# Kernel optimization log

Measured on AMD Instinct MI355X. Metric: run time of the kernel, lower is better.

The kernel has to match this reference:

```python
import jax, jax.numpy as jnp
import numpy as np

EMBED_DIM = 768
NUM_HEADS = 8
HEAD_DIM = EMBED_DIM // NUM_HEADS


def setup_inputs() -> dict:
    key = jax.random.key(0)
    ks = jax.random.split(key, 10)
    B, N_m, N_p = 8, 1024, 1024
    s = 1.0 / np.sqrt(EMBED_DIM)
    inp = {
        "mammo_tokens": jax.random.normal(ks[0], (B, N_m, EMBED_DIM), jnp.float32),
        "patho_tokens": jax.random.normal(ks[1], (B, N_p, EMBED_DIM), jnp.float32),
        "q_w": jax.random.uniform(ks[2], (EMBED_DIM, EMBED_DIM), jnp.float32, -s, s),
        "q_b": jax.random.uniform(ks[3], (EMBED_DIM,), jnp.float32, -s, s),
        "k_w": jax.random.uniform(ks[4], (EMBED_DIM, EMBED_DIM), jnp.float32, -s, s),
        "k_b": jax.random.uniform(ks[5], (EMBED_DIM,), jnp.float32, -s, s),
        "v_w": jax.random.uniform(ks[6], (EMBED_DIM, EMBED_DIM), jnp.float32, -s, s),
        "v_b": jax.random.uniform(ks[7], (EMBED_DIM,), jnp.float32, -s, s),
        "o_w": jax.random.uniform(ks[8], (EMBED_DIM, EMBED_DIM), jnp.float32, -s, s),
        "o_b": jax.random.uniform(ks[9], (EMBED_DIM,), jnp.float32, -s, s),
    }
    return inp


def reference(mammo_tokens, patho_tokens, q_w, q_b, k_w, k_b, v_w, v_b, o_w, o_b):
    B, N_m, E = mammo_tokens.shape
    N_p = patho_tokens.shape[1]
    H, D = NUM_HEADS, HEAD_DIM
    # torch Linear: y = x @ W^T + b
    Q = (mammo_tokens @ q_w.T + q_b).reshape(B, N_m, H, D)
    K = (patho_tokens @ k_w.T + k_b).reshape(B, N_p, H, D)
    V = (patho_tokens @ v_w.T + v_b).reshape(B, N_p, H, D)
    # scores: [B, H, N_m, N_p]
    scores = jnp.einsum("bmhd,bphd->bhmp", Q, K) / np.sqrt(D).astype(jnp.float32)
    attn = jax.nn.softmax(scores, axis=-1)  # dropout omitted (eval mode)
    attended = jnp.einsum("bhmp,bphd->bmhd", attn, V).reshape(B, N_m, E)
    attended = attended @ o_w.T + o_b
    attn_avg = attn.mean(axis=1)  # [B, N_m, N_p]
    return attended, attn_avg
```

## Files before the change

kernel.cpp:

```cpp
#include <hip/hip_runtime.h>

typedef short short4v __attribute__((ext_vector_type(4)));
typedef short short8 __attribute__((ext_vector_type(8)));
typedef float f32x4 __attribute__((ext_vector_type(4)));

__device__ __forceinline__ f32x4 mfma16(short8 a, short8 b, f32x4 c) {
    return __builtin_amdgcn_mfma_f32_16x16x32_bf16(a, b, c, 0, 0, 0);
}
__device__ __forceinline__ short f2bs(float f) {
    __bf16 h = (__bf16)f;
    return __builtin_bit_cast(short, h);
}
__device__ __forceinline__ void gld_lds16(const void* g, void* l) {
    __builtin_amdgcn_global_load_lds(
        (const __attribute__((address_space(1))) void*)g,
        (__attribute__((address_space(3))) void*)l, 16, 0, 0);
}

__global__ __launch_bounds__(256) void cvt_b16(const float* __restrict__ in,
                                               short* __restrict__ out) {
    const size_t i = ((size_t)blockIdx.x * 256 + threadIdx.x) * 8;
    const float4 v0 = *(const float4*)(in + i);
    const float4 v1 = *(const float4*)(in + i + 4);
    short8 s;
    s[0] = f2bs(v0.x); s[1] = f2bs(v0.y); s[2] = f2bs(v0.z); s[3] = f2bs(v0.w);
    s[4] = f2bs(v1.x); s[5] = f2bs(v1.y); s[6] = f2bs(v1.z); s[7] = f2bs(v1.w);
    *(short8*)(out + i) = s;
}

__global__ __launch_bounds__(256) void gemm_bw(const short* __restrict__ A,
                                               const short* __restrict__ Wb,
                                               const float* __restrict__ bias,
                                               void* __restrict__ Cv,
                                               int mode) {
    __shared__ short sBuf[2][128][64];

    const int tid = threadIdx.x;
    const int wave = tid >> 6, lane = tid & 63;
    const int quad = lane >> 4, l16 = lane & 15;
    const int n0 = blockIdx.x * 128;
    const int r0 = blockIdx.y * 128;
    const int wm = (wave & 1) * 64;
    const int wn = (wave >> 1) * 64;

    const int lrow   = lane >> 3;
    const int lchunk = (lane & 7) ^ lrow;
    const short* Abase =
        A + (size_t)(r0 + wave * 32 + lrow) * 768 + lchunk * 8;
    const short* Wbase =
        Wb + (size_t)(n0 + wave * 32 + lrow) * 768 + lchunk * 8;

    f32x4 acc[4][4];
#pragma unroll
    for (int mt = 0; mt < 4; ++mt)
#pragma unroll
        for (int nt = 0; nt < 4; ++nt) acc[mt][nt] = (f32x4){0.f, 0.f, 0.f, 0.f};

    for (int k0 = 0; k0 < 768; k0 += 64) {
        __syncthreads();

#pragma unroll
        for (int i = 0; i < 4; ++i) {
            gld_lds16(Abase + k0 + (size_t)i * 8 * 768,
                      &sBuf[0][(wave * 4 + i) * 8][0]);
            gld_lds16(Wbase + k0 + (size_t)i * 8 * 768,
                      &sBuf[1][(wave * 4 + i) * 8][0]);
        }

        __syncthreads();

#pragma unroll
        for (int ks = 0; ks < 2; ++ks) {
            short8 af[4], bf[4];
#pragma unroll
            for (int mt = 0; mt < 4; ++mt)
                af[mt] = *(const short8*)
                    &sBuf[0][wm + mt * 16 + l16][((ks * 4 + quad) ^ (l16 & 7)) * 8];
#pragma unroll
            for (int nt = 0; nt < 4; ++nt)
                bf[nt] = *(const short8*)
                    &sBuf[1][wn + nt * 16 + l16][((ks * 4 + quad) ^ (l16 & 7)) * 8];
#pragma unroll
            for (int mt = 0; mt < 4; ++mt)
#pragma unroll
                for (int nt = 0; nt < 4; ++nt)
                    acc[mt][nt] = mfma16(af[mt], bf[nt], acc[mt][nt]);
        }
    }

    short* Cs = (short*)Cv;

    if (mode == 1) {
        short* tl = &sBuf[0][0][0];
        const int b_  = r0 >> 10;
        const int p0v = r0 & 1023;
#pragma unroll 1
        for (int pass = 0; pass < 2; ++pass) {
            __syncthreads();
            if ((wave >> 1) == pass) {
#pragma unroll
                for (int nt = 0; nt < 4; ++nt) {
                    const float bv = bias[n0 + wn + nt * 16 + l16];
#pragma unroll
                    for (int mt = 0; mt < 4; ++mt) {
                        short4v pk;
#pragma unroll
                        for (int rr = 0; rr < 4; ++rr)
                            pk[rr] = f2bs(acc[mt][nt][rr] + bv);
                        *(short4v*)&tl[(nt * 16 + l16) * 132 + wm + mt * 16 +
                                       quad * 4] = pk;
                    }
                }
            }
            __syncthreads();
            const int row = tid >> 2, seg = tid & 3;
            const int n_g = n0 + pass * 64 + row;
            short* dst = Cs + ((size_t)(b_ * 768 + n_g) << 10) + p0v + seg * 32;
            const short* srcl = &tl[row * 132 + seg * 32];
#pragma unroll
            for (int u = 0; u < 4; ++u)
                *(short8*)(dst + u * 8) = *(const short8*)(srcl + u * 8);
        }
        return;
    }

#pragma unroll
    for (int nt = 0; nt < 4; ++nt) {
        const int n = n0 + wn + nt * 16 + l16;
        const float bv = bias[n];
        const size_t hcb = (size_t)((n / 96) * 12 + ((n % 96) >> 3)) * 65536 +
                           (n % 8);
#pragma unroll
        for (int mt = 0; mt < 4; ++mt) {
#pragma unroll
            for (int rr = 0; rr < 4; ++rr) {
                const int row = r0 + wm + mt * 16 + quad * 4 + rr;
                Cs[hcb + (size_t)row * 8] = f2bs(acc[mt][nt][rr] + bv);
            }
        }
    }
}

__global__ __launch_bounds__(256) void gemm_mfma(const short* __restrict__ A,
                                                 const float* __restrict__ W,
                                                 const float* __restrict__ bias,
                                                 void* __restrict__ Cv,
                                                 int mode) {
    __shared__ short sBuf[2][128][64];

    const int tid = threadIdx.x;
    const int wave = tid >> 6, lane = tid & 63;
    const int quad = lane >> 4, l16 = lane & 15;
    const int n0 = blockIdx.x * 128;
    const int r0 = blockIdx.y * 128;
    const int wm = (wave & 1) * 64;
    const int wn = (wave >> 1) * 64;

    const int lrow   = lane >> 3;
    const int lchunk = (lane & 7) ^ lrow;
    const short* Abase =
        A + (size_t)(r0 + wave * 32 + lrow) * 768 + lchunk * 8;

    const int wrow = tid >> 1;
    const int wseg = tid & 1;
    const float* Wbase = W + (size_t)(n0 + wrow) * 768 + wseg * 32;
    const int wsw = wrow & 7;

    f32x4 acc[4][4];
#pragma unroll
    for (int mt = 0; mt < 4; ++mt)
#pragma unroll
        for (int nt = 0; nt < 4; ++nt) acc[mt][nt] = (f32x4){0.f, 0.f, 0.f, 0.f};

    for (int k0 = 0; k0 < 768; k0 += 64) {
        float4 wv[8];
#pragma unroll
        for (int j = 0; j < 8; ++j)
            wv[j] = *(const float4*)(Wbase + k0 + j * 4);

        __syncthreads();

#pragma unroll
        for (int i = 0; i < 4; ++i)
            gld_lds16(Abase + k0 + (size_t)i * 8 * 768,
                      &sBuf[0][(wave * 4 + i) * 8][0]);

#pragma unroll
        for (int c = 0; c < 4; ++c) {
            const float4 a = wv[2 * c], b = wv[2 * c + 1];
            short8 p;
            p[0] = f2bs(a.x); p[1] = f2bs(a.y); p[2] = f2bs(a.z); p[3] = f2bs(a.w);
            p[4] = f2bs(b.x); p[5] = f2bs(b.y); p[6] = f2bs(b.z); p[7] = f2bs(b.w);
            *(short8*)&sBuf[1][wrow][((wseg * 4 + c) ^ wsw) * 8] = p;
        }

        __syncthreads();

#pragma unroll
        for (int ks = 0; ks < 2; ++ks) {
            short8 af[4], bf[4];
#pragma unroll
            for (int mt = 0; mt < 4; ++mt)
                af[mt] = *(const short8*)
                    &sBuf[0][wm + mt * 16 + l16][((ks * 4 + quad) ^ (l16 & 7)) * 8];
#pragma unroll
            for (int nt = 0; nt < 4; ++nt)
                bf[nt] = *(const short8*)
                    &sBuf[1][wn + nt * 16 + l16][((ks * 4 + quad) ^ (l16 & 7)) * 8];
#pragma unroll
            for (int mt = 0; mt < 4; ++mt)
#pragma unroll
                for (int nt = 0; nt < 4; ++nt)
                    acc[mt][nt] = mfma16(af[mt], bf[nt], acc[mt][nt]);
        }
    }

    float* Cf = (float*)Cv;
#pragma unroll
    for (int nt = 0; nt < 4; ++nt) {
        const int n = n0 + wn + nt * 16 + l16;
        const float bv = bias[n];
#pragma unroll
        for (int mt = 0; mt < 4; ++mt) {
#pragma unroll
            for (int rr = 0; rr < 4; ++rr) {
                const int row = r0 + wm + mt * 16 + quad * 4 + rr;
                Cf[(size_t)row * 768 + n] = acc[mt][nt][rr] + bv;
            }
        }
    }
}

__global__ __launch_bounds__(256) void flash_att(const short* __restrict__ QH,
                                                 const short* __restrict__ KH,
                                                 const short* __restrict__ Vt,
                                                 short* __restrict__ att,
                                                 float* __restrict__ linv) {
    __shared__ short sKp[2][12][64][8];
    __shared__ short sV[2][96][8][8];
    __shared__ short Pl[4][32][76];

    const int h  = blockIdx.x;
    const int mt = blockIdx.y;
    const int b  = blockIdx.z;
    const int tid  = threadIdx.x;
    const int wave = tid >> 6;
    const int lane = tid & 63;
    const int quad = lane >> 4;
    const int l16  = lane & 15;

    const int m0 = mt * 128 + wave * 32;
    const size_t brow = (size_t)b * 1024;
    const float scale = 0.1020620726159657f;

    short8 aq[2][3];
#pragma unroll
    for (int mf = 0; mf < 2; ++mf)
#pragma unroll
        for (int kc = 0; kc < 3; ++kc)
            aq[mf][kc] = *(const short8*)(QH +
                ((size_t)(h * 12 + kc * 4 + quad) * 8192 + brow + m0 +
                 mf * 16 + l16) * 8);

    const short* kp_[3];
#pragma unroll
    for (int i = 0; i < 3; ++i)
        kp_[i] = KH + ((size_t)(h * 12 + wave * 3 + i) * 8192 + brow + lane) * 8;

    const short* vp_[3];
#pragma unroll
    for (int i = 0; i < 3; ++i) {
        const int slot = i * 256 + tid;
        const int row = slot >> 3;
        const int g = (slot & 7) ^ (row & 7);
        vp_[i] = Vt + ((size_t)b * 768 + h * 96 + row) * 1024 + g * 8;
    }

    int vB[2];
#pragma unroll
    for (int kv = 0; kv < 2; ++kv)
        vB[kv] = l16 * 64 + (((kv * 4 + quad) ^ (l16 & 7)) * 8);

    f32x4 o[2][6];
#pragma unroll
    for (int mf = 0; mf < 2; ++mf)
#pragma unroll
        for (int nt = 0; nt < 6; ++nt) o[mf][nt] = (f32x4){0.f, 0.f, 0.f, 0.f};
    float li[2][4] = {};

#define FA_STAGE(BUF)                                                          \
    {                                                                          \
        _Pragma("unroll")                                                      \
        for (int i = 0; i < 3; ++i) {                                          \
            gld_lds16(kp_[i], &sKp[BUF][wave * 3 + i][0][0]);                  \
            kp_[i] += 512;                                                     \
        }                                                                      \
        _Pragma("unroll")                                                      \
        for (int i = 0; i < 3; ++i) {                                          \
            gld_lds16(vp_[i], (short*)sV[BUF] + (i * 256 + wave * 64) * 8);    \
            vp_[i] += 64;                                                      \
        }                                                                      \
    }

    FA_STAGE(0)
    __syncthreads();

    int cur = 0;
#pragma unroll 1
    for (int t = 0; t < 16; ++t) {
        if (t < 15) FA_STAGE(cur ^ 1)

#pragma unroll
        for (int j = 0; j < 4; ++j) {
            short8 kf[3];
#pragma unroll
            for (int kc = 0; kc < 3; ++kc)
                kf[kc] = *(const short8*)((const short*)sKp[cur] +
                    ((kc * 4 + quad) * 64 + j * 16 + l16) * 8);
            f32x4 s0 = (f32x4){0.f, 0.f, 0.f, 0.f};
            f32x4 s1 = (f32x4){0.f, 0.f, 0.f, 0.f};
            s0 = mfma16(aq[0][0], kf[0], s0);
            s1 = mfma16(aq[1][0], kf[0], s1);
            s0 = mfma16(aq[0][1], kf[1], s0);
            s1 = mfma16(aq[1][1], kf[1], s1);
            s0 = mfma16(aq[0][2], kf[2], s0);
            s1 = mfma16(aq[1][2], kf[2], s1);
#pragma unroll
            for (int r = 0; r < 4; ++r) {
                const float e0 = __expf(s0[r] * scale);
                const float e1 = __expf(s1[r] * scale);
                li[0][r] += e0;
                li[1][r] += e1;
                Pl[wave][quad * 4 + r][j * 16 + l16]      = f2bs(e0);
                Pl[wave][16 + quad * 4 + r][j * 16 + l16] = f2bs(e1);
            }
        }

        __builtin_amdgcn_s_waitcnt(0xc07f);

        short8 ap[2][2];
#pragma unroll
        for (int mf = 0; mf < 2; ++mf)
#pragma unroll
            for (int kv = 0; kv < 2; ++kv)
                ap[mf][kv] = *(const short8*)
                    &Pl[wave][mf * 16 + l16][kv * 32 + quad * 8];

#pragma unroll
        for (int nt = 0; nt < 6; ++nt) {
#pragma unroll
            for (int kv = 0; kv < 2; ++kv) {
                const short8 v =
                    *(const short8*)((const short*)sV[cur] + nt * 1024 + vB[kv]);
                o[0][nt] = mfma16(ap[0][kv], v, o[0][nt]);
                o[1][nt] = mfma16(ap[1][kv], v, o[1][nt]);
            }
        }

        __syncthreads();
        cur ^= 1;
    }
#undef FA_STAGE

#pragma unroll
    for (int mf = 0; mf < 2; ++mf) {
        float inv[4];
#pragma unroll
        for (int r = 0; r < 4; ++r) {
#pragma unroll
            for (int off = 1; off < 16; off <<= 1)
                li[mf][r] += __shfl_xor(li[mf][r], off, 16);
            inv[r] = 1.0f / li[mf][r];
        }
#pragma unroll
        for (int nt = 0; nt < 6; ++nt)
#pragma unroll
            for (int r = 0; r < 4; ++r)
                att[(brow + m0 + mf * 16 + quad * 4 + r) * 768 + h * 96 +
                    nt * 16 + l16] = f2bs(o[mf][nt][r] * inv[r]);
        if (l16 == 0) {
#pragma unroll
            for (int r = 0; r < 4; ++r)
                linv[(((size_t)b * 8 + h) << 10) + m0 + mf * 16 + quad * 4 + r] =
                    inv[r];
        }
    }
}

__global__ __launch_bounds__(256) void attn_avg6(const short* __restrict__ QH,
                                                 const short* __restrict__ KH,
                                                 const float* __restrict__ linv,
                                                 float* __restrict__ avg) {
    __shared__ short sQ[12][128][8];
    __shared__ short sK[12][128][8];

    const int pt = blockIdx.x;
    const int mt = blockIdx.y;
    const int b  = blockIdx.z;
    const int tid  = threadIdx.x;
    const int wave = tid >> 6;
    const int lane = tid & 63;
    const int quad = lane >> 4;
    const int l16  = lane & 15;

    const int m0 = mt * 128;
    const int p0 = pt * 128;
    const size_t brow = (size_t)b * 1024;
    const int wm = (wave & 1) * 64;
    const int wn = (wave >> 1) * 64;
    const float scale2 = 0.14724445f;

    const size_t qoff = (size_t)(brow + m0 + lane) * 8;
    const size_t koff = (size_t)(brow + p0 + lane) * 8;
    const float* Lb_  = linv + (((size_t)b * 8) << 10) + m0 + wm + quad * 4;

    f32x4 acc[4][4];
#pragma unroll
    for (int x = 0; x < 4; ++x)
#pragma unroll
        for (int y = 0; y < 4; ++y) acc[x][y] = (f32x4){0.f, 0.f, 0.f, 0.f};

#pragma unroll 1
    for (int h = 0; h < 8; ++h) {
        __syncthreads();

#pragma unroll
        for (int i = 0; i < 6; ++i) {
            const int j = wave * 6 + i;
            const int c = j >> 1, half = j & 1;
            const size_t pl = (size_t)(h * 12 + c) * 65536 + half * 512;
            gld_lds16(QH + pl + qoff, &sQ[c][half * 64][0]);
            gld_lds16(KH + pl + koff, &sK[c][half * 64][0]);
        }

        f32x4 il[4];
#pragma unroll
        for (int x = 0; x < 4; ++x)
            il[x] = 0.125f * *(const f32x4*)(Lb_ + ((size_t)h << 10) + x * 16);

        __syncthreads();

        short8 af[4][3], bf[4][3];
#pragma unroll
        for (int x = 0; x < 4; ++x)
#pragma unroll
            for (int kc = 0; kc < 3; ++kc) {
                af[x][kc] = *(const short8*)&sQ[kc * 4 + quad][wm + x * 16 + l16][0];
                bf[x][kc] = *(const short8*)&sK[kc * 4 + quad][wn + x * 16 + l16][0];
            }

#pragma unroll
        for (int x = 0; x < 4; ++x)
#pragma unroll
            for (int y = 0; y < 4; ++y) {
                f32x4 s = (f32x4){0.f, 0.f, 0.f, 0.f};
                s = mfma16(af[x][0], bf[y][0], s);
                s = mfma16(af[x][1], bf[y][1], s);
                s = mfma16(af[x][2], bf[y][2], s);
#pragma unroll
                for (int r = 0; r < 4; ++r)
                    acc[x][y][r] += __builtin_exp2f(s[r] * scale2) * il[x][r];
            }
    }

#pragma unroll
    for (int x = 0; x < 4; ++x)
#pragma unroll
        for (int y = 0; y < 4; ++y)
#pragma unroll
            for (int r = 0; r < 4; ++r)
                avg[(brow + m0 + wm + x * 16 + quad * 4 + r) * 1024 +
                    p0 + wn + y * 16 + l16] = acc[x][y][r];
}

extern "C" void kernel_launch(void* const* d_in, const int* in_sizes, int n_in,
                              void* d_out, int out_size, void* d_ws, size_t ws_size,
                              hipStream_t stream) {
    (void)in_sizes; (void)n_in; (void)out_size; (void)d_ws; (void)ws_size;

    float* mam = (float*)d_in[0];
    float* pat = (float*)d_in[1];
    const float* qw = (const float*)d_in[2];
    const float* qb = (const float*)d_in[3];
    const float* kw = (const float*)d_in[4];
    const float* kb = (const float*)d_in[5];
    const float* vw = (const float*)d_in[6];
    const float* vb = (const float*)d_in[7];
    const float* ow = (const float*)d_in[8];
    const float* ob = (const float*)d_in[9];

    const size_t NTOK = (size_t)8 * 1024 * 768;
    const size_t NW   = (size_t)768 * 768;
    float* out_att = (float*)d_out;
    float* out_avg = out_att + NTOK;

    short* Am = (short*)d_out;
    short* Ap = (short*)out_avg;
    short* Qh = (short*)mam;
    short* Kh = Qh + NTOK;
    short* Vt = (short*)pat;
    short* Ab = Vt + NTOK;
    float* LV = (float*)(Am + NTOK);
    short* WQ = (short*)(LV + 65536);
    short* WK = WQ + NW;
    short* WV = WK + NW;

    dim3 bb(256), gg(6, 64);
    cvt_b16<<<3072, bb, 0, stream>>>(mam, Am);
    cvt_b16<<<3072, bb, 0, stream>>>(pat, Ap);
    cvt_b16<<<288, bb, 0, stream>>>(qw, WQ);
    cvt_b16<<<288, bb, 0, stream>>>(kw, WK);
    cvt_b16<<<288, bb, 0, stream>>>(vw, WV);

    gemm_bw<<<gg, bb, 0, stream>>>(Am, WQ, qb, Qh, 3);
    gemm_bw<<<gg, bb, 0, stream>>>(Ap, WK, kb, Kh, 3);
    gemm_bw<<<gg, bb, 0, stream>>>(Ap, WV, vb, Vt, 1);

    flash_att<<<dim3(8, 8, 8), bb, 0, stream>>>(Qh, Kh, Vt, Ab, LV);
    attn_avg6<<<dim3(8, 8, 8), bb, 0, stream>>>(Qh, Kh, LV, out_avg);

    gemm_mfma<<<gg, bb, 0, stream>>>(Ab, ow, ob, out_att, 2);
}
```

Before: 294.8 us.

## Double-buffer attn_avg Q/K staging and route output projection through bf16 gemm_bw

The attention-average kernel now stages Q/K head planes in 4-plane chunks into a double-buffered LDS array, prefetching the next chunk while MFMAs run on the current one. Before, it loaded all 12 planes per head and then synchronized. Separately, the output projection drops the fp32-weight gemm_mfma kernel. The o_w weights are pre-converted to bf16 into the freed Qh buffer and the shared gemm_bw kernel is reused with a new fp32-output mode 2. This trades an extra conversion launch and more barriers for overlapping loads with compute and removing per-tile weight conversion.

```diff
diff --git a/kernel.cpp b/kernel.cpp
--- a/kernel.cpp
+++ b/kernel.cpp
@@ -124,6 +124,24 @@
         return;
     }
 
+    if (mode == 2) {
+        float* Cf = (float*)Cv;
+#pragma unroll
+        for (int nt = 0; nt < 4; ++nt) {
+            const int n = n0 + wn + nt * 16 + l16;
+            const float bv = bias[n];
+#pragma unroll
+            for (int mt = 0; mt < 4; ++mt) {
+#pragma unroll
+                for (int rr = 0; rr < 4; ++rr) {
+                    const int row = r0 + wm + mt * 16 + quad * 4 + rr;
+                    Cf[(size_t)row * 768 + n] = acc[mt][nt][rr] + bv;
+                }
+            }
+        }
+        return;
+    }
+
 #pragma unroll
     for (int nt = 0; nt < 4; ++nt) {
         const int n = n0 + wn + nt * 16 + l16;
@@ -136,96 +154,6 @@
             for (int rr = 0; rr < 4; ++rr) {
                 const int row = r0 + wm + mt * 16 + quad * 4 + rr;
                 Cs[hcb + (size_t)row * 8] = f2bs(acc[mt][nt][rr] + bv);
-            }
-        }
-    }
-}
-
-__global__ __launch_bounds__(256) void gemm_mfma(const short* __restrict__ A,
-                                                 const float* __restrict__ W,
-                                                 const float* __restrict__ bias,
-                                                 void* __restrict__ Cv,
-                                                 int mode) {
-    __shared__ short sBuf[2][128][64];
-
-    const int tid = threadIdx.x;
-    const int wave = tid >> 6, lane = tid & 63;
-    const int quad = lane >> 4, l16 = lane & 15;
-    const int n0 = blockIdx.x * 128;
-    const int r0 = blockIdx.y * 128;
-    const int wm = (wave & 1) * 64;
-    const int wn = (wave >> 1) * 64;
-
-    const int lrow   = lane >> 3;
-    const int lchunk = (lane & 7) ^ lrow;
-    const short* Abase =
-        A + (size_t)(r0 + wave * 32 + lrow) * 768 + lchunk * 8;
-
-    const int wrow = tid >> 1;
-    const int wseg = tid & 1;
-    const float* Wbase = W + (size_t)(n0 + wrow) * 768 + wseg * 32;
-    const int wsw = wrow & 7;
-
-    f32x4 acc[4][4];
-#pragma unroll
-    for (int mt = 0; mt < 4; ++mt)
-#pragma unroll
-        for (int nt = 0; nt < 4; ++nt) acc[mt][nt] = (f32x4){0.f, 0.f, 0.f, 0.f};
-
-    for (int k0 = 0; k0 < 768; k0 += 64) {
-        float4 wv[8];
-#pragma unroll
-        for (int j = 0; j < 8; ++j)
-            wv[j] = *(const float4*)(Wbase + k0 + j * 4);
-
-        __syncthreads();
-
-#pragma unroll
-        for (int i = 0; i < 4; ++i)
-            gld_lds16(Abase + k0 + (size_t)i * 8 * 768,
-                      &sBuf[0][(wave * 4 + i) * 8][0]);
-
-#pragma unroll
-        for (int c = 0; c < 4; ++c) {
-            const float4 a = wv[2 * c], b = wv[2 * c + 1];
-            short8 p;
-            p[0] = f2bs(a.x); p[1] = f2bs(a.y); p[2] = f2bs(a.z); p[3] = f2bs(a.w);
-            p[4] = f2bs(b.x); p[5] = f2bs(b.y); p[6] = f2bs(b.z); p[7] = f2bs(b.w);
-            *(short8*)&sBuf[1][wrow][((wseg * 4 + c) ^ wsw) * 8] = p;
-        }
-
-        __syncthreads();
-
-#pragma unroll
-        for (int ks = 0; ks < 2; ++ks) {
-            short8 af[4], bf[4];
-#pragma unroll
-            for (int mt = 0; mt < 4; ++mt)
-                af[mt] = *(const short8*)
-                    &sBuf[0][wm + mt * 16 + l16][((ks * 4 + quad) ^ (l16 & 7)) * 8];
-#pragma unroll
-            for (int nt = 0; nt < 4; ++nt)
-                bf[nt] = *(const short8*)
-                    &sBuf[1][wn + nt * 16 + l16][((ks * 4 + quad) ^ (l16 & 7)) * 8];
-#pragma unroll
-            for (int mt = 0; mt < 4; ++mt)
-#pragma unroll
-                for (int nt = 0; nt < 4; ++nt)
-                    acc[mt][nt] = mfma16(af[mt], bf[nt], acc[mt][nt]);
-        }
-    }
-
-    float* Cf = (float*)Cv;
-#pragma unroll
-    for (int nt = 0; nt < 4; ++nt) {
-        const int n = n0 + wn + nt * 16 + l16;
-        const float bv = bias[n];
-#pragma unroll
-        for (int mt = 0; mt < 4; ++mt) {
-#pragma unroll
-            for (int rr = 0; rr < 4; ++rr) {
-                const int row = r0 + wm + mt * 16 + quad * 4 + rr;
-                Cf[(size_t)row * 768 + n] = acc[mt][nt][rr] + bv;
             }
         }
     }
@@ -387,12 +315,11 @@
     }
 }
 
-__global__ __launch_bounds__(256) void attn_avg6(const short* __restrict__ QH,
+__global__ __launch_bounds__(256) void attn_avg7(const short* __restrict__ QH,
                                                  const short* __restrict__ KH,
                                                  const float* __restrict__ linv,
                                                  float* __restrict__ avg) {
-    __shared__ short sQ[12][128][8];
-    __shared__ short sK[12][128][8];
+    __shared__ short sT[2][2][4][128][8];
 
     const int pt = blockIdx.x;
     const int mt = blockIdx.y;
@@ -410,9 +337,20 @@
     const int wn = (wave >> 1) * 64;
     const float scale2 = 0.14724445f;
 
-    const size_t qoff = (size_t)(brow + m0 + lane) * 8;
-    const size_t koff = (size_t)(brow + p0 + lane) * 8;
-    const float* Lb_  = linv + (((size_t)b * 8) << 10) + m0 + wm + quad * 4;
+    const int tensor = wave >> 1;
+    const short* srcp[4];
+    int dsto[4];
+#pragma unroll
+    for (int i = 0; i < 4; ++i) {
+        const int plane = (wave & 1) * 2 + (i >> 1);
+        const int half  = i & 1;
+        const short* base = tensor ? KH : QH;
+        const int r0_ = tensor ? p0 : m0;
+        srcp[i] = base + ((size_t)plane * 8192 + brow + r0_ + half * 64 + lane) * 8;
+        dsto[i] = ((tensor * 4 + plane) * 128 + half * 64) * 8;
+    }
+
+    const float* Lb_ = linv + (((size_t)b * 8) << 10) + m0 + wm + quad * 4;
 
     f32x4 acc[4][4];
 #pragma unroll
@@ -420,48 +358,68 @@
 #pragma unroll
         for (int y = 0; y < 4; ++y) acc[x][y] = (f32x4){0.f, 0.f, 0.f, 0.f};
 
+#define AV_STAGE(BUF)                                                          \
+    {                                                                          \
+        short* bb_ = (short*)sT + (BUF) * 8192;                                \
+        _Pragma("unroll")                                                      \
+        for (int i = 0; i < 4; ++i) {                                          \
+            gld_lds16(srcp[i], bb_ + dsto[i]);                                 \
+            srcp[i] += 262144;                    \
+        }                                                                      \
+    }
+
+    AV_STAGE(0)
+    __syncthreads();
+
+    int cur = 0;
 #pragma unroll 1
     for (int h = 0; h < 8; ++h) {
-        __syncthreads();
-
-#pragma unroll
-        for (int i = 0; i < 6; ++i) {
-            const int j = wave * 6 + i;
-            const int c = j >> 1, half = j & 1;
-            const size_t pl = (size_t)(h * 12 + c) * 65536 + half * 512;
-            gld_lds16(QH + pl + qoff, &sQ[c][half * 64][0]);
-            gld_lds16(KH + pl + koff, &sK[c][half * 64][0]);
-        }
-
         f32x4 il[4];
 #pragma unroll
         for (int x = 0; x < 4; ++x)
             il[x] = 0.125f * *(const f32x4*)(Lb_ + ((size_t)h << 10) + x * 16);
 
-        __syncthreads();
-
-        short8 af[4][3], bf[4][3];
+        f32x4 s[4][4];
 #pragma unroll
         for (int x = 0; x < 4; ++x)
 #pragma unroll
-            for (int kc = 0; kc < 3; ++kc) {
-                af[x][kc] = *(const short8*)&sQ[kc * 4 + quad][wm + x * 16 + l16][0];
-                bf[x][kc] = *(const short8*)&sK[kc * 4 + quad][wn + x * 16 + l16][0];
-            }
-
-#pragma unroll
-        for (int x = 0; x < 4; ++x)
-#pragma unroll
-            for (int y = 0; y < 4; ++y) {
-                f32x4 s = (f32x4){0.f, 0.f, 0.f, 0.f};
-                s = mfma16(af[x][0], bf[y][0], s);
-                s = mfma16(af[x][1], bf[y][1], s);
-                s = mfma16(af[x][2], bf[y][2], s);
-#pragma unroll
-                for (int r = 0; r < 4; ++r)
-                    acc[x][y][r] += __builtin_exp2f(s[r] * scale2) * il[x][r];
-            }
-    }
+            for (int y = 0; y < 4; ++y) s[x][y] = (f32x4){0.f, 0.f, 0.f, 0.f};
+
+#pragma unroll
+        for (int kc = 0; kc < 3; ++kc) {
+            if (kc != 2 || h != 7) AV_STAGE(cur ^ 1)
+
+            const short* qb = (const short*)sT + cur * 8192 + quad * 1024;
+            const short* kb = qb + 4096;
+            short8 af[4], bf[4];
+#pragma unroll
+            for (int x = 0; x < 4; ++x)
+                af[x] = *(const short8*)(qb + (wm + x * 16 + l16) * 8);
+#pragma unroll
+            for (int y = 0; y < 4; ++y)
+                bf[y] = *(const short8*)(kb + (wn + y * 16 + l16) * 8);
+#pragma unroll
+            for (int x = 0; x < 4; ++x)
+#pragma unroll
+                for (int y = 0; y < 4; ++y)
+                    s[x][y] = mfma16(af[x], bf[y], s[x][y]);
+
+            if (kc == 2) {
+#pragma unroll
+                for (int x = 0; x < 4; ++x)
+#pragma unroll
+                    for (int y = 0; y < 4; ++y)
+#pragma unroll
+                        for (int r = 0; r < 4; ++r)
+                            acc[x][y][r] +=
+                                __builtin_exp2f(s[x][y][r] * scale2) * il[x][r];
+            }
+
+            __syncthreads();
+            cur ^= 1;
+        }
+    }
+#undef AV_STAGE
 
 #pragma unroll
     for (int x = 0; x < 4; ++x)
@@ -504,6 +462,7 @@
     short* WQ = (short*)(LV + 65536);
     short* WK = WQ + NW;
     short* WV = WK + NW;
+    short* WO = Qh;
 
     dim3 bb(256), gg(6, 64);
     cvt_b16<<<3072, bb, 0, stream>>>(mam, Am);
@@ -517,7 +476,8 @@
     gemm_bw<<<gg, bb, 0, stream>>>(Ap, WV, vb, Vt, 1);
 
     flash_att<<<dim3(8, 8, 8), bb, 0, stream>>>(Qh, Kh, Vt, Ab, LV);
-    attn_avg6<<<dim3(8, 8, 8), bb, 0, stream>>>(Qh, Kh, LV, out_avg);
-
-    gemm_mfma<<<gg, bb, 0, stream>>>(Ab, ow, ob, out_att, 2);
-}
+    attn_avg7<<<dim3(8, 8, 8), bb, 0, stream>>>(Qh, Kh, LV, out_avg);
+
+    cvt_b16<<<288, bb, 0, stream>>>(ow, WO);
+    gemm_bw<<<gg, bb, 0, stream>>>(Ab, WO, ob, out_att, 2);
+}
```

Result: faster. 282.1 us (-4.3%).
